# Kernel optimization log

Hardware: AMD Instinct MI355X
Metric: run time of the kernel (lower is better)

## Reference

```python
import jax, jax.numpy as jnp
import numpy as np

H = 8
D_MODEL = 512
NEG = -1e9  # fp32 masking value from the torch source


def setup_inputs() -> dict:
    key = jax.random.key(0)
    ks = jax.random.split(key, 13)
    B, T, C, D = 2, 512, 8, D_MODEL
    s = 1.0 / np.sqrt(D)
    inp = {
        "query": jax.random.normal(ks[0], (B, T, C, D), jnp.float32),
        "key": jax.random.normal(ks[1], (B, T, C, D), jnp.float32),
        "value": jax.random.normal(ks[2], (B, T, C, D), jnp.float32),
        "mask": jax.random.randint(ks[3], (B, T, T, 1), 0, 2, jnp.int32),
        # four Linear(d_model, d_model) layers, stored as (in, out)
        "Wq": jax.random.normal(ks[4], (D, D), jnp.float32) * s,
        "bq": jax.random.normal(ks[5], (D,), jnp.float32) * s,
        "Wk": jax.random.normal(ks[6], (D, D), jnp.float32) * s,
        "bk": jax.random.normal(ks[7], (D,), jnp.float32) * s,
        "Wv": jax.random.normal(ks[8], (D, D), jnp.float32) * s,
        "bv": jax.random.normal(ks[9], (D,), jnp.float32) * s,
        "Wo": jax.random.normal(ks[10], (D, D), jnp.float32) * s,
        "bo": jax.random.normal(ks[11], (D,), jnp.float32) * s,
    }
    return inp


def _mha(query, key, value, mask, Wq, bq, Wk, bk, Wv, bv, Wo, bo):
    B, T, C, D = query.shape
    h, dk = H, D // H

    def proj(x, W, b):
        y = (x @ W + b).reshape(B, T, C, h, dk)
        return jnp.transpose(y, (0, 3, 2, 1, 4))  # [B,h,C,T,dk] (torch transpose(1,3))

    q = proj(query, Wq, bq)
    k = proj(key, Wk, bk)
    v = proj(value, Wv, bv)

    scores = jnp.einsum("bhctd,bhcsd->bhcts", q, k) / np.sqrt(dk)  # [B,h,C,T,T]
    # The torch view/transpose/view dance is just a permutation putting C last;
    # it is equivalent to masking scores[b,h,c,t,s] where mask[b,t,s,0]==0
    # (mask broadcast over heads h and channels c).
    m = mask[:, :, :, 0]  # [B,T,Tk]
    scores = jnp.where(m[:, None, None, :, :] == 0, NEG, scores)
    p_attn = jax.nn.softmax(scores, axis=-1)
    # dropout omitted (inference/deterministic reference)
    x = jnp.einsum("bhcts,bhcsd->bhctd", p_attn, v)  # [B,h,C,T,dk]
    x = jnp.transpose(x, (0, 3, 2, 1, 4)).reshape(B, T, C, D)
    return x @ Wo + bo


def reference(query, key, value, mask, Wq, bq, Wk, bk, Wv, bv, Wo, bo):
    return _mha(query, key, value, mask, Wq, bq, Wk, bk, Wv, bv, Wo, bo)
```

## Files before the change

kernel.cpp:

```cpp
#include <hip/hip_runtime.h>
#include <hip/hip_bf16.h>

typedef __bf16 bf16;
typedef __bf16 bf16x8 __attribute__((ext_vector_type(8)));
typedef float floatx4 __attribute__((ext_vector_type(4)));


#define AS1 __attribute__((address_space(1)))
#define AS3 __attribute__((address_space(3)))

__device__ __forceinline__ void gload_lds16(const bf16* g, bf16* l) {
    __builtin_amdgcn_global_load_lds((const AS1 unsigned int*)g,
                                     (AS3 unsigned int*)l, 16, 0, 0);
}

union Pack8 { bf16 h[8]; uint4 u; };
union Pack4 { bf16 h[4]; unsigned long long u; };

__global__ __launch_bounds__(256) void wtr_kernel(
    const float* __restrict__ Wq, const float* __restrict__ Wk,
    const float* __restrict__ Wv, const float* __restrict__ Wo,
    bf16* __restrict__ WT)
{
    __shared__ float Ts[64][65];
    const int tid = threadIdx.x;
    const int k0 = blockIdx.x * 64;
    const int n0 = blockIdx.y * 64;
    const int z  = blockIdx.z;
    const float* W = (z == 0) ? Wq : (z == 1) ? Wk : (z == 2) ? Wv : Wo;
    bf16* O = WT + (size_t)z * 512 * 512;
    #pragma unroll
    for (int i = 0; i < 16; i++) {
        const int r = i * 4 + (tid >> 6), c = tid & 63;
        Ts[r][c] = W[(size_t)(k0 + r) * 512 + n0 + c];
    }
    __syncthreads();
    #pragma unroll
    for (int i = 0; i < 16; i++) {
        const int a = i * 4 + (tid >> 6), c = tid & 63;
        O[(size_t)(n0 + a) * 512 + k0 + c] = (bf16)Ts[c][a];
    }
}

__global__ __launch_bounds__(512, 4) void gemm_qkv(
    const float* __restrict__ Aq, const float* __restrict__ Ak,
    const float* __restrict__ Av, const bf16* __restrict__ WT,
    const float* __restrict__ Bq, const float* __restrict__ Bk,
    const float* __restrict__ Bv,
    bf16* __restrict__ Oq, bf16* __restrict__ Ok, bf16* __restrict__ Ov)
{
    __shared__ bf16 Asm[128 * 32];
    __shared__ bf16 Bsm[128 * 32];
    __shared__ bf16 Tsm[128][136];
    const int z = blockIdx.z;
    const float* A    = (z == 0) ? Aq : (z == 1) ? Ak : Av;
    const float* bias = (z == 0) ? Bq : (z == 1) ? Bk : Bv;
    bf16* out         = (z == 0) ? Oq : (z == 1) ? Ok : Ov;
    const bf16* BT = WT + (size_t)z * 262144;
    const float scale = (z == 0) ? 0.125f : 1.0f;

    const int tid  = threadIdx.x;
    const int lane = tid & 63;
    const int wave = tid >> 6;
    const int quad = lane >> 4;
    const int l16  = lane & 15;
    const int mblk = blockIdx.x * 128;
    const int nblk = blockIdx.y * 128;

    const int srow = wave * 16 + (lane >> 2);
    const int scol = (lane & 3) * 8;
    const float* Ag = A + (size_t)(mblk + srow) * 512 + scol;
    const bf16* Bg  = BT + (size_t)(nblk + srow) * 512 + scol;
    bf16* Alp = Asm + srow * 32 + scol;
    bf16* Bl  = Bsm + wave * 16 * 32;

    const int wr = (wave >> 1) * 32;
    const int wc = (wave & 1) * 64;

    floatx4 acc[2][4] = {};
    for (int k0 = 0; k0 < 512; k0 += 32) {
        gload_lds16(Bg + k0, Bl);
        float4 x0 = *(const float4*)(Ag + k0);
        float4 x1 = *(const float4*)(Ag + k0 + 4);
        Pack8 pa;
        pa.h[0] = (bf16)x0.x; pa.h[1] = (bf16)x0.y;
        pa.h[2] = (bf16)x0.z; pa.h[3] = (bf16)x0.w;
        pa.h[4] = (bf16)x1.x; pa.h[5] = (bf16)x1.y;
        pa.h[6] = (bf16)x1.z; pa.h[7] = (bf16)x1.w;
        *(uint4*)Alp = pa.u;
        __syncthreads();
        bf16x8 a[2], b[4];
        #pragma unroll
        for (int mt = 0; mt < 2; mt++)
            a[mt] = *(const bf16x8*)(Asm + (wr + mt * 16 + l16) * 32 + quad * 8);
        #pragma unroll
        for (int nt = 0; nt < 4; nt++)
            b[nt] = *(const bf16x8*)(Bsm + (wc + nt * 16 + l16) * 32 + quad * 8);
        #pragma unroll
        for (int mt = 0; mt < 2; mt++)
            #pragma unroll
            for (int nt = 0; nt < 4; nt++)
                acc[mt][nt] = __builtin_amdgcn_mfma_f32_16x16x32_bf16(
                    a[mt], b[nt], acc[mt][nt], 0, 0, 0);
        __syncthreads();
    }

    if (z != 2) {
        #pragma unroll
        for (int mt = 0; mt < 2; mt++) {
            #pragma unroll
            for (int nt = 0; nt < 4; nt++) {
                const int colg = nblk + wc + nt * 16 + l16;
                const float bb = bias[colg];
                #pragma unroll
                for (int r = 0; r < 4; r++) {
                    const int rowg = mblk + wr + mt * 16 + quad * 4 + r;
                    const float v = (acc[mt][nt][r] + bb) * scale;
                    const int b_ = rowg >> 12;
                    const int t_ = (rowg >> 3) & 511;
                    const int c  = rowg & 7;
                    const int h  = colg >> 6;
                    const int d  = colg & 63;
                    const int hd = b_ * 64 + h * 8 + c;
                    out[((size_t)hd * 512 + t_) * 64 + d] = (bf16)v;
                }
            }
        }
    } else {
        #pragma unroll
        for (int mt = 0; mt < 2; mt++) {
            #pragma unroll
            for (int nt = 0; nt < 4; nt++) {
                const int cl = wc + nt * 16 + l16;
                const float bb = bias[nblk + cl];
                #pragma unroll
                for (int r = 0; r < 4; r++)
                    Tsm[wr + mt * 16 + quad * 4 + r][cl] =
                        (bf16)(acc[mt][nt][r] + bb);
            }
        }
        __syncthreads();
        const int b_ = mblk >> 12;
        const int t0 = (mblk >> 3) & 511;
        #pragma unroll
        for (int ch = tid; ch < 1024; ch += 512) {
            const int col = ch >> 3, c = ch & 7;
            const int h = (nblk + col) >> 6, d = (nblk + col) & 63;
            const int hd = b_ * 64 + h * 8 + c;
            Pack8 lo, hi;
            #pragma unroll
            for (int j = 0; j < 8; j++) lo.h[j] = Tsm[j * 8 + c][col];
            #pragma unroll
            for (int j = 0; j < 8; j++) hi.h[j] = Tsm[(j + 8) * 8 + c][col];
            bf16* dst = out + ((size_t)hd * 64 + d) * 512 + t0;
            *(uint4*)dst = lo.u;
            *(uint4*)(dst + 8) = hi.u;
        }
    }
}

__global__ __launch_bounds__(512, 4) void gemm_o(
    const bf16* __restrict__ A, const bf16* __restrict__ BT,
    const float* __restrict__ bias, float* __restrict__ out)
{
    __shared__ bf16 Asm[128 * 32];
    __shared__ bf16 Bsm[128 * 32];
    const int tid  = threadIdx.x;
    const int lane = tid & 63;
    const int wave = tid >> 6;
    const int quad = lane >> 4;
    const int l16  = lane & 15;
    const int mblk = blockIdx.x * 128;
    const int nblk = blockIdx.y * 128;

    const int srow = wave * 16 + (lane >> 2);
    const int scol = (lane & 3) * 8;
    const bf16* Ag = A + (size_t)(mblk + srow) * 512 + scol;
    const bf16* Bg = BT + (size_t)(nblk + srow) * 512 + scol;
    bf16* Al = Asm + wave * 16 * 32;
    bf16* Bl = Bsm + wave * 16 * 32;

    const int wr = (wave >> 1) * 32;
    const int wc = (wave & 1) * 64;

    floatx4 acc[2][4] = {};
    for (int k0 = 0; k0 < 512; k0 += 32) {
        gload_lds16(Ag + k0, Al);
        gload_lds16(Bg + k0, Bl);
        __syncthreads();
        bf16x8 a[2], b[4];
        #pragma unroll
        for (int mt = 0; mt < 2; mt++)
            a[mt] = *(const bf16x8*)(Asm + (wr + mt * 16 + l16) * 32 + quad * 8);
        #pragma unroll
        for (int nt = 0; nt < 4; nt++)
            b[nt] = *(const bf16x8*)(Bsm + (wc + nt * 16 + l16) * 32 + quad * 8);
        #pragma unroll
        for (int mt = 0; mt < 2; mt++)
            #pragma unroll
            for (int nt = 0; nt < 4; nt++)
                acc[mt][nt] = __builtin_amdgcn_mfma_f32_16x16x32_bf16(
                    a[mt], b[nt], acc[mt][nt], 0, 0, 0);
        __syncthreads();
    }

    #pragma unroll
    for (int mt = 0; mt < 2; mt++) {
        #pragma unroll
        for (int nt = 0; nt < 4; nt++) {
            const int colg = nblk + wc + nt * 16 + l16;
            const float bb = bias[colg];
            #pragma unroll
            for (int r = 0; r < 4; r++) {
                const int rowg = mblk + wr + mt * 16 + quad * 4 + r;
                out[(size_t)rowg * 512 + colg] = acc[mt][nt][r] + bb;
            }
        }
    }
}

#define PST 520

__global__ __launch_bounds__(256, 2) void attn_kernel(
    const bf16* __restrict__ Qws, const bf16* __restrict__ Kws,
    const bf16* __restrict__ Vtws, const int* __restrict__ mask,
    bf16* __restrict__ Xws)
{
    __shared__ bf16 Psm[64][PST];
    __shared__ float redM[4][64];
    __shared__ float redS[4][64];
    const int tid  = threadIdx.x;
    const int wave = tid >> 6;
    const int lane = tid & 63;
    const int quad = lane >> 4;
    const int l16  = lane & 15;
    const int s_ = blockIdx.x;
    const int o_ = ((s_ & 7) << 7) | (s_ >> 3);
    const int hd = o_ >> 3;
    const int qt = o_ & 7;
    const int q0 = qt * 64;
    const int b = hd >> 6;
    const int h = (hd >> 3) & 7;
    const int c = hd & 7;

    const bf16* Qh = Qws + (size_t)hd * 512 * 64;
    const bf16* Kh = Kws + (size_t)hd * 512 * 64;
    const int* mp = mask + ((size_t)b * 512 + q0) * 512;

    bf16x8 aq[4][2];
    #pragma unroll
    for (int s = 0; s < 4; s++) {
        aq[s][0] = *(const bf16x8*)(Qh + (size_t)(q0 + s * 16 + l16) * 64 + quad * 8);
        aq[s][1] = *(const bf16x8*)(Qh + (size_t)(q0 + s * 16 + l16) * 64 + 32 + quad * 8);
    }

    floatx4 sv[4][8];
    #pragma unroll
    for (int s = 0; s < 4; s++)
        #pragma unroll
        for (int nt = 0; nt < 8; nt++)
            sv[s][nt] = (floatx4){0.f, 0.f, 0.f, 0.f};

    #pragma unroll
    for (int nt = 0; nt < 8; nt++) {
        const int s0 = wave * 128 + nt * 16;
        bf16x8 bk0 = *(const bf16x8*)(Kh + (size_t)(s0 + l16) * 64 + quad * 8);
        bf16x8 bk1 = *(const bf16x8*)(Kh + (size_t)(s0 + l16) * 64 + 32 + quad * 8);
        #pragma unroll
        for (int s = 0; s < 4; s++) {
            sv[s][nt] = __builtin_amdgcn_mfma_f32_16x16x32_bf16(
                bk0, aq[s][0], sv[s][nt], 0, 0, 0);
            sv[s][nt] = __builtin_amdgcn_mfma_f32_16x16x32_bf16(
                bk1, aq[s][1], sv[s][nt], 0, 0, 0);
        }
    }

    float mx[4] = {-3.0e38f, -3.0e38f, -3.0e38f, -3.0e38f};
    #pragma unroll
    for (int s = 0; s < 4; s++)
        #pragma unroll
        for (int nt = 0; nt < 8; nt++) {
            const int4 mv = *(const int4*)(
                mp + (size_t)(s * 16 + l16) * 512 + wave * 128 + nt * 16 + quad * 4);
            float v0 = sv[s][nt][0] + ((mv.x == 0) ? -1.0e9f : 0.0f);
            float v1 = sv[s][nt][1] + ((mv.y == 0) ? -1.0e9f : 0.0f);
            float v2 = sv[s][nt][2] + ((mv.z == 0) ? -1.0e9f : 0.0f);
            float v3 = sv[s][nt][3] + ((mv.w == 0) ? -1.0e9f : 0.0f);
            sv[s][nt][0] = v0; sv[s][nt][1] = v1;
            sv[s][nt][2] = v2; sv[s][nt][3] = v3;
            mx[s] = fmaxf(mx[s], fmaxf(fmaxf(v0, v1), fmaxf(v2, v3)));
        }
    #pragma unroll
    for (int s = 0; s < 4; s++) {
        mx[s] = fmaxf(mx[s], __shfl_xor(mx[s], 16, 64));
        mx[s] = fmaxf(mx[s], __shfl_xor(mx[s], 32, 64));
    }
    if (quad == 0)
        #pragma unroll
        for (int s = 0; s < 4; s++) redM[wave][s * 16 + l16] = mx[s];
    __syncthreads();

    float mf[4], sum[4] = {0.f, 0.f, 0.f, 0.f};
    #pragma unroll
    for (int s = 0; s < 4; s++) {
        const int qr = s * 16 + l16;
        mf[s] = fmaxf(fmaxf(redM[0][qr], redM[1][qr]),
                      fmaxf(redM[2][qr], redM[3][qr]));
    }
    #pragma unroll
    for (int s = 0; s < 4; s++)
        #pragma unroll
        for (int nt = 0; nt < 8; nt++)
            #pragma unroll
            for (int r = 0; r < 4; r++) {
                const float e = __expf(sv[s][nt][r] - mf[s]);
                sv[s][nt][r] = e;
                sum[s] += e;
            }
    #pragma unroll
    for (int s = 0; s < 4; s++) {
        sum[s] += __shfl_xor(sum[s], 16, 64);
        sum[s] += __shfl_xor(sum[s], 32, 64);
    }
    if (quad == 0)
        #pragma unroll
        for (int s = 0; s < 4; s++) redS[wave][s * 16 + l16] = sum[s];
    __syncthreads();

    float inv[4];
    #pragma unroll
    for (int s = 0; s < 4; s++) {
        const int qr = s * 16 + l16;
        inv[s] = 1.f / (redS[0][qr] + redS[1][qr] + redS[2][qr] + redS[3][qr]);
    }
    #pragma unroll
    for (int s = 0; s < 4; s++)
        #pragma unroll
        for (int nt = 0; nt < 8; nt++) {
            Pack4 pk;
            #pragma unroll
            for (int r = 0; r < 4; r++)
                pk.h[r] = (bf16)(sv[s][nt][r] * inv[s]);
            *(unsigned long long*)&Psm[s * 16 + l16][wave * 128 + nt * 16 + quad * 4]
                = pk.u;
        }
    __syncthreads();

    const bf16* Vh = Vtws + (size_t)hd * 64 * 512;
    const int d0 = wave * 16;
    floatx4 o[4] = {};
    #pragma unroll
    for (int ks = 0; ks < 16; ks++) {
        bf16x8 bv = *(const bf16x8*)(Vh + (size_t)(d0 + l16) * 512 + ks * 32 + quad * 8);
        #pragma unroll
        for (int rt = 0; rt < 4; rt++) {
            bf16x8 ap = *(const bf16x8*)(&Psm[rt * 16 + l16][ks * 32 + quad * 8]);
            o[rt] = __builtin_amdgcn_mfma_f32_16x16x32_bf16(ap, bv, o[rt], 0, 0, 0);
        }
    }
    #pragma unroll
    for (int rt = 0; rt < 4; rt++)
        #pragma unroll
        for (int r = 0; r < 4; r++) {
            const int q = q0 + rt * 16 + quad * 4 + r;
            const size_t row = ((size_t)b * 512 + q) * 8 + c;
            Xws[row * 512 + h * 64 + d0 + l16] = (bf16)o[rt][r];
        }
}

extern "C" void kernel_launch(void* const* d_in, const int* in_sizes, int n_in,
                              void* d_out, int out_size, void* d_ws, size_t ws_size,
                              hipStream_t stream)
{
    const float* qin  = (const float*)d_in[0];
    const float* kin  = (const float*)d_in[1];
    const float* vin  = (const float*)d_in[2];
    const int*   mask = (const int*)d_in[3];
    const float* Bq = (const float*)d_in[5];
    const float* Bk = (const float*)d_in[7];
    const float* Bv = (const float*)d_in[9];
    const float* Bo = (const float*)d_in[11];
    float* out = (float*)d_out;

    const size_t R = (size_t)8192 * 512;
    bf16* r0 = (bf16*)d_ws;
    bf16* r1 = r0 + R;
    bf16* r2 = r1 + R;
    bf16* r3 = r2 + R;
    bf16* WT = r3 + R;

    wtr_kernel<<<dim3(8, 8, 4), dim3(256), 0, stream>>>(
        (const float*)d_in[4], (const float*)d_in[6],
        (const float*)d_in[8], (const float*)d_in[10], WT);
    gemm_qkv<<<dim3(64, 4, 3), dim3(512), 0, stream>>>(
        qin, kin, vin, WT, Bq, Bk, Bv, r0, r1, r2);
    attn_kernel<<<dim3(1024), dim3(256), 0, stream>>>(
        r0, r1, r2, mask, r3);
    gemm_o<<<dim3(64, 4), dim3(512), 0, stream>>>(
        r3, WT + (size_t)3 * 262144, Bo, out);
}
```

Measured before the change: 193.5 us.

## Double-buffer LDS and register-prefetch tiles in QKV and output GEMMs

Replaces the single-buffered global_load_lds loop in both projection GEMMs with a fully unrolled, double-buffered LDS pipeline. Global loads for tile t+2 are issued into registers while tile t is computed, and custom lgkmcnt+barrier asm replaces __syncthreads. The aim is to hide global-load latency behind MFMA work. In exchange it uses more LDS and registers, and it drops the direct-to-LDS loads in favour of register staging.

```diff
diff --git a/kernel.cpp b/kernel.cpp
--- a/kernel.cpp
+++ b/kernel.cpp
@@ -6,16 +6,17 @@
 typedef float floatx4 __attribute__((ext_vector_type(4)));
 
 
-#define AS1 __attribute__((address_space(1)))
-#define AS3 __attribute__((address_space(3)))
-
-__device__ __forceinline__ void gload_lds16(const bf16* g, bf16* l) {
-    __builtin_amdgcn_global_load_lds((const AS1 unsigned int*)g,
-                                     (AS3 unsigned int*)l, 16, 0, 0);
-}
-
 union Pack8 { bf16 h[8]; uint4 u; };
 union Pack4 { bf16 h[4]; unsigned long long u; };
+
+__device__ __forceinline__ void store_pack8(bf16* dst, float4 a, float4 b) {
+    Pack8 p;
+    p.h[0] = (bf16)a.x; p.h[1] = (bf16)a.y; p.h[2] = (bf16)a.z; p.h[3] = (bf16)a.w;
+    p.h[4] = (bf16)b.x; p.h[5] = (bf16)b.y; p.h[6] = (bf16)b.z; p.h[7] = (bf16)b.w;
+    *(uint4*)dst = p.u;
+}
+
+#define BAR_LG asm volatile("s_waitcnt lgkmcnt(0)\n\ts_barrier" ::: "memory")
 
 __global__ __launch_bounds__(256) void wtr_kernel(
     const float* __restrict__ Wq, const float* __restrict__ Wk,
@@ -49,9 +50,12 @@
     const float* __restrict__ Bv,
     bf16* __restrict__ Oq, bf16* __restrict__ Ok, bf16* __restrict__ Ov)
 {
-    __shared__ bf16 Asm[128 * 32];
-    __shared__ bf16 Bsm[128 * 32];
-    __shared__ bf16 Tsm[128][136];
+    __shared__ __align__(16) bf16 smem[17408];
+    bf16* Ab0 = smem;
+    bf16* Ab1 = smem + 4096;
+    bf16* Bb0 = smem + 8192;
+    bf16* Bb1 = smem + 12288;
+
     const int z = blockIdx.z;
     const float* A    = (z == 0) ? Aq : (z == 1) ? Ak : Av;
     const float* bias = (z == 0) ? Bq : (z == 1) ? Bk : Bv;
@@ -71,38 +75,68 @@
     const int scol = (lane & 3) * 8;
     const float* Ag = A + (size_t)(mblk + srow) * 512 + scol;
     const bf16* Bg  = BT + (size_t)(nblk + srow) * 512 + scol;
-    bf16* Alp = Asm + srow * 32 + scol;
-    bf16* Bl  = Bsm + wave * 16 * 32;
+    const int aoff = srow * 32 + scol;
 
     const int wr = (wave >> 1) * 32;
     const int wc = (wave & 1) * 64;
 
     floatx4 acc[2][4] = {};
-    for (int k0 = 0; k0 < 512; k0 += 32) {
-        gload_lds16(Bg + k0, Bl);
-        float4 x0 = *(const float4*)(Ag + k0);
-        float4 x1 = *(const float4*)(Ag + k0 + 4);
-        Pack8 pa;
-        pa.h[0] = (bf16)x0.x; pa.h[1] = (bf16)x0.y;
-        pa.h[2] = (bf16)x0.z; pa.h[3] = (bf16)x0.w;
-        pa.h[4] = (bf16)x1.x; pa.h[5] = (bf16)x1.y;
-        pa.h[6] = (bf16)x1.z; pa.h[7] = (bf16)x1.w;
-        *(uint4*)Alp = pa.u;
-        __syncthreads();
+
+    float4 ax0 = *(const float4*)(Ag);
+    float4 ax1 = *(const float4*)(Ag + 4);
+    uint4  bx  = *(const uint4*)(Bg);
+    store_pack8(Ab0 + aoff, ax0, ax1);
+    *(uint4*)(Bb0 + aoff) = bx;
+    float4 ay0 = *(const float4*)(Ag + 32);
+    float4 ay1 = *(const float4*)(Ag + 36);
+    uint4  by  = *(const uint4*)(Bg + 32);
+    store_pack8(Ab1 + aoff, ay0, ay1);
+    *(uint4*)(Bb1 + aoff) = by;
+    ax0 = *(const float4*)(Ag + 64);
+    ax1 = *(const float4*)(Ag + 68);
+    bx  = *(const uint4*)(Bg + 64);
+    BAR_LG;
+
+    #pragma unroll
+    for (int t = 0; t < 16; t++) {
+        bf16* Ab = (t & 1) ? Ab1 : Ab0;
+        bf16* Bb = (t & 1) ? Bb1 : Bb0;
         bf16x8 a[2], b[4];
         #pragma unroll
         for (int mt = 0; mt < 2; mt++)
-            a[mt] = *(const bf16x8*)(Asm + (wr + mt * 16 + l16) * 32 + quad * 8);
+            a[mt] = *(const bf16x8*)(Ab + (wr + mt * 16 + l16) * 32 + quad * 8);
         #pragma unroll
         for (int nt = 0; nt < 4; nt++)
-            b[nt] = *(const bf16x8*)(Bsm + (wc + nt * 16 + l16) * 32 + quad * 8);
+            b[nt] = *(const bf16x8*)(Bb + (wc + nt * 16 + l16) * 32 + quad * 8);
         #pragma unroll
         for (int mt = 0; mt < 2; mt++)
             #pragma unroll
             for (int nt = 0; nt < 4; nt++)
                 acc[mt][nt] = __builtin_amdgcn_mfma_f32_16x16x32_bf16(
                     a[mt], b[nt], acc[mt][nt], 0, 0, 0);
-        __syncthreads();
+        if (t <= 12) {
+            const int kL = (t + 3) * 32;
+            if (t & 1) {
+                ax0 = *(const float4*)(Ag + kL);
+                ax1 = *(const float4*)(Ag + kL + 4);
+                bx  = *(const uint4*)(Bg + kL);
+            } else {
+                ay0 = *(const float4*)(Ag + kL);
+                ay1 = *(const float4*)(Ag + kL + 4);
+                by  = *(const uint4*)(Bg + kL);
+            }
+        }
+        if (t <= 13) {
+            BAR_LG;
+            if (t & 1) {
+                store_pack8(Ab + aoff, ay0, ay1);
+                *(uint4*)(Bb + aoff) = by;
+            } else {
+                store_pack8(Ab + aoff, ax0, ax1);
+                *(uint4*)(Bb + aoff) = bx;
+            }
+            BAR_LG;
+        }
     }
 
     if (z != 2) {
@@ -127,6 +161,9 @@
             }
         }
     } else {
+        __syncthreads();
+        typedef bf16 TsmRow[136];
+        TsmRow* Tsm = (TsmRow*)smem;
         #pragma unroll
         for (int mt = 0; mt < 2; mt++) {
             #pragma unroll
@@ -163,8 +200,12 @@
     const bf16* __restrict__ A, const bf16* __restrict__ BT,
     const float* __restrict__ bias, float* __restrict__ out)
 {
-    __shared__ bf16 Asm[128 * 32];
-    __shared__ bf16 Bsm[128 * 32];
+    __shared__ __align__(16) bf16 smem[16384];
+    bf16* Ab0 = smem;
+    bf16* Ab1 = smem + 4096;
+    bf16* Bb0 = smem + 8192;
+    bf16* Bb1 = smem + 12288;
+
     const int tid  = threadIdx.x;
     const int lane = tid & 63;
     const int wave = tid >> 6;
@@ -177,31 +218,53 @@
     const int scol = (lane & 3) * 8;
     const bf16* Ag = A + (size_t)(mblk + srow) * 512 + scol;
     const bf16* Bg = BT + (size_t)(nblk + srow) * 512 + scol;
-    bf16* Al = Asm + wave * 16 * 32;
-    bf16* Bl = Bsm + wave * 16 * 32;
+    const int aoff = srow * 32 + scol;
 
     const int wr = (wave >> 1) * 32;
     const int wc = (wave & 1) * 64;
 
     floatx4 acc[2][4] = {};
-    for (int k0 = 0; k0 < 512; k0 += 32) {
-        gload_lds16(Ag + k0, Al);
-        gload_lds16(Bg + k0, Bl);
-        __syncthreads();
+
+    uint4 xa = *(const uint4*)(Ag);
+    uint4 xb = *(const uint4*)(Bg);
+    *(uint4*)(Ab0 + aoff) = xa;
+    *(uint4*)(Bb0 + aoff) = xb;
+    uint4 ya = *(const uint4*)(Ag + 32);
+    uint4 yb = *(const uint4*)(Bg + 32);
+    *(uint4*)(Ab1 + aoff) = ya;
+    *(uint4*)(Bb1 + aoff) = yb;
+    xa = *(const uint4*)(Ag + 64);
+    xb = *(const uint4*)(Bg + 64);
+    BAR_LG;
+
+    #pragma unroll
+    for (int t = 0; t < 16; t++) {
+        bf16* Ab = (t & 1) ? Ab1 : Ab0;
+        bf16* Bb = (t & 1) ? Bb1 : Bb0;
         bf16x8 a[2], b[4];
         #pragma unroll
         for (int mt = 0; mt < 2; mt++)
-            a[mt] = *(const bf16x8*)(Asm + (wr + mt * 16 + l16) * 32 + quad * 8);
+            a[mt] = *(const bf16x8*)(Ab + (wr + mt * 16 + l16) * 32 + quad * 8);
         #pragma unroll
         for (int nt = 0; nt < 4; nt++)
-            b[nt] = *(const bf16x8*)(Bsm + (wc + nt * 16 + l16) * 32 + quad * 8);
+            b[nt] = *(const bf16x8*)(Bb + (wc + nt * 16 + l16) * 32 + quad * 8);
         #pragma unroll
         for (int mt = 0; mt < 2; mt++)
             #pragma unroll
             for (int nt = 0; nt < 4; nt++)
                 acc[mt][nt] = __builtin_amdgcn_mfma_f32_16x16x32_bf16(
                     a[mt], b[nt], acc[mt][nt], 0, 0, 0);
-        __syncthreads();
+        if (t <= 12) {
+            const int kL = (t + 3) * 32;
+            if (t & 1) { xa = *(const uint4*)(Ag + kL); xb = *(const uint4*)(Bg + kL); }
+            else       { ya = *(const uint4*)(Ag + kL); yb = *(const uint4*)(Bg + kL); }
+        }
+        if (t <= 13) {
+            BAR_LG;
+            if (t & 1) { *(uint4*)(Ab + aoff) = ya; *(uint4*)(Bb + aoff) = yb; }
+            else       { *(uint4*)(Ab + aoff) = xa; *(uint4*)(Bb + aoff) = xb; }
+            BAR_LG;
+        }
     }
 
     #pragma unroll
```

Measured after the change: 195.4 us. No clear change (+1.0%).

## Retile QKV GEMM to full-width 64-row blocks and shrink output GEMM tiles

Applied to the files above, without the earlier changes.

The QKV projection now gives each block 64 rows across all 512 output columns. Each fp32 input row is therefore read and converted to bf16 once instead of four times. The V transpose epilogue is staged through a shared buffer reused in four column chunks. The output GEMM switches to 64x128 tiles with 256 threads, doubling the block count for better CU occupancy. The risks are more accumulator registers per thread, lower occupancy from the larger shared footprint, and extra syncs in the V epilogue.

```diff
diff --git a/kernel.cpp b/kernel.cpp
--- a/kernel.cpp
+++ b/kernel.cpp
@@ -16,6 +16,12 @@
 
 union Pack8 { bf16 h[8]; uint4 u; };
 union Pack4 { bf16 h[4]; unsigned long long u; };
+
+__device__ __forceinline__ void store_pack4(bf16* dst, float4 a) {
+    Pack4 p;
+    p.h[0] = (bf16)a.x; p.h[1] = (bf16)a.y; p.h[2] = (bf16)a.z; p.h[3] = (bf16)a.w;
+    *(unsigned long long*)dst = p.u;
+}
 
 __global__ __launch_bounds__(256) void wtr_kernel(
     const float* __restrict__ Wq, const float* __restrict__ Wk,
@@ -42,16 +48,17 @@
     }
 }
 
-__global__ __launch_bounds__(512, 4) void gemm_qkv(
+__global__ __launch_bounds__(512, 3) void gemm_qkv(
     const float* __restrict__ Aq, const float* __restrict__ Ak,
     const float* __restrict__ Av, const bf16* __restrict__ WT,
     const float* __restrict__ Bq, const float* __restrict__ Bk,
     const float* __restrict__ Bv,
     bf16* __restrict__ Oq, bf16* __restrict__ Ok, bf16* __restrict__ Ov)
 {
-    __shared__ bf16 Asm[128 * 32];
-    __shared__ bf16 Bsm[128 * 32];
-    __shared__ bf16 Tsm[128][136];
+    __shared__ __align__(16) bf16 smem[18432];
+    bf16* Asm = smem;
+    bf16* Bsm = smem + 2048;
+
     const int z = blockIdx.z;
     const float* A    = (z == 0) ? Aq : (z == 1) ? Ak : Av;
     const float* bias = (z == 0) ? Bq : (z == 1) ? Bk : Bv;
@@ -64,40 +71,36 @@
     const int wave = tid >> 6;
     const int quad = lane >> 4;
     const int l16  = lane & 15;
-    const int mblk = blockIdx.x * 128;
-    const int nblk = blockIdx.y * 128;
-
-    const int srow = wave * 16 + (lane >> 2);
-    const int scol = (lane & 3) * 8;
-    const float* Ag = A + (size_t)(mblk + srow) * 512 + scol;
-    const bf16* Bg  = BT + (size_t)(nblk + srow) * 512 + scol;
-    bf16* Alp = Asm + srow * 32 + scol;
-    bf16* Bl  = Bsm + wave * 16 * 32;
-
-    const int wr = (wave >> 1) * 32;
-    const int wc = (wave & 1) * 64;
-
-    floatx4 acc[2][4] = {};
+    const int mblk = blockIdx.x * 64;
+
+    const int arow = tid >> 3;
+    const int acol = (tid & 7) * 4;
+    const float* Ag = A + (size_t)(mblk + arow) * 512 + acol;
+    const int aoff = arow * 32 + acol;
+    const int srowB = wave * 16 + (lane >> 2);
+    const int scolB = (lane & 3) * 8;
+    const bf16* Bg = BT + (size_t)srowB * 512 + scolB;
+    bf16* Bl = Bsm + wave * 16 * 32;
+
+    const int wc = wave * 64;
+
+    floatx4 acc[4][4] = {};
     for (int k0 = 0; k0 < 512; k0 += 32) {
-        gload_lds16(Bg + k0, Bl);
-        float4 x0 = *(const float4*)(Ag + k0);
-        float4 x1 = *(const float4*)(Ag + k0 + 4);
-        Pack8 pa;
-        pa.h[0] = (bf16)x0.x; pa.h[1] = (bf16)x0.y;
-        pa.h[2] = (bf16)x0.z; pa.h[3] = (bf16)x0.w;
-        pa.h[4] = (bf16)x1.x; pa.h[5] = (bf16)x1.y;
-        pa.h[6] = (bf16)x1.z; pa.h[7] = (bf16)x1.w;
-        *(uint4*)Alp = pa.u;
+        #pragma unroll
+        for (int i = 0; i < 4; i++)
+            gload_lds16(Bg + (size_t)i * 128 * 512 + k0, Bl + i * 128 * 32);
+        float4 x = *(const float4*)(Ag + k0);
+        store_pack4(Asm + aoff, x);
         __syncthreads();
-        bf16x8 a[2], b[4];
-        #pragma unroll
-        for (int mt = 0; mt < 2; mt++)
-            a[mt] = *(const bf16x8*)(Asm + (wr + mt * 16 + l16) * 32 + quad * 8);
+        bf16x8 a[4], b[4];
+        #pragma unroll
+        for (int mt = 0; mt < 4; mt++)
+            a[mt] = *(const bf16x8*)(Asm + (mt * 16 + l16) * 32 + quad * 8);
         #pragma unroll
         for (int nt = 0; nt < 4; nt++)
             b[nt] = *(const bf16x8*)(Bsm + (wc + nt * 16 + l16) * 32 + quad * 8);
         #pragma unroll
-        for (int mt = 0; mt < 2; mt++)
+        for (int mt = 0; mt < 4; mt++)
             #pragma unroll
             for (int nt = 0; nt < 4; nt++)
                 acc[mt][nt] = __builtin_amdgcn_mfma_f32_16x16x32_bf16(
@@ -107,14 +110,14 @@
 
     if (z != 2) {
         #pragma unroll
-        for (int mt = 0; mt < 2; mt++) {
+        for (int mt = 0; mt < 4; mt++) {
             #pragma unroll
             for (int nt = 0; nt < 4; nt++) {
-                const int colg = nblk + wc + nt * 16 + l16;
+                const int colg = wc + nt * 16 + l16;
                 const float bb = bias[colg];
                 #pragma unroll
                 for (int r = 0; r < 4; r++) {
-                    const int rowg = mblk + wr + mt * 16 + quad * 4 + r;
+                    const int rowg = mblk + mt * 16 + quad * 4 + r;
                     const float v = (acc[mt][nt][r] + bb) * scale;
                     const int b_ = rowg >> 12;
                     const int t_ = (rowg >> 3) & 511;
@@ -127,66 +130,76 @@
             }
         }
     } else {
-        #pragma unroll
-        for (int mt = 0; mt < 2; mt++) {
-            #pragma unroll
-            for (int nt = 0; nt < 4; nt++) {
-                const int cl = wc + nt * 16 + l16;
-                const float bb = bias[nblk + cl];
-                #pragma unroll
-                for (int r = 0; r < 4; r++)
-                    Tsm[wr + mt * 16 + quad * 4 + r][cl] =
-                        (bf16)(acc[mt][nt][r] + bb);
-            }
-        }
         __syncthreads();
+        typedef bf16 TsmRow[136];
+        TsmRow* Tsm = (TsmRow*)smem;
         const int b_ = mblk >> 12;
         const int t0 = (mblk >> 3) & 511;
         #pragma unroll
-        for (int ch = tid; ch < 1024; ch += 512) {
-            const int col = ch >> 3, c = ch & 7;
-            const int h = (nblk + col) >> 6, d = (nblk + col) & 63;
-            const int hd = b_ * 64 + h * 8 + c;
-            Pack8 lo, hi;
-            #pragma unroll
-            for (int j = 0; j < 8; j++) lo.h[j] = Tsm[j * 8 + c][col];
-            #pragma unroll
-            for (int j = 0; j < 8; j++) hi.h[j] = Tsm[(j + 8) * 8 + c][col];
-            bf16* dst = out + ((size_t)hd * 64 + d) * 512 + t0;
-            *(uint4*)dst = lo.u;
-            *(uint4*)(dst + 8) = hi.u;
-        }
-    }
-}
-
-__global__ __launch_bounds__(512, 4) void gemm_o(
+        for (int cb = 0; cb < 4; cb++) {
+            if ((wave >> 1) == cb) {
+                #pragma unroll
+                for (int mt = 0; mt < 4; mt++) {
+                    #pragma unroll
+                    for (int nt = 0; nt < 4; nt++) {
+                        const int colg = wc + nt * 16 + l16;
+                        const int cl = colg - cb * 128;
+                        const float bb = bias[colg];
+                        #pragma unroll
+                        for (int r = 0; r < 4; r++)
+                            Tsm[mt * 16 + quad * 4 + r][cl] =
+                                (bf16)(acc[mt][nt][r] + bb);
+                    }
+                }
+            }
+            __syncthreads();
+            #pragma unroll
+            for (int e = tid; e < 1024; e += 512) {
+                const int col = e >> 3, c = e & 7;
+                const int gcol = cb * 128 + col;
+                const int h = gcol >> 6, d = gcol & 63;
+                const int hd = b_ * 64 + h * 8 + c;
+                Pack8 pk;
+                #pragma unroll
+                for (int j = 0; j < 8; j++) pk.h[j] = Tsm[j * 8 + c][col];
+                *(uint4*)(out + ((size_t)hd * 64 + d) * 512 + t0) = pk.u;
+            }
+            __syncthreads();
+        }
+    }
+}
+
+__global__ __launch_bounds__(256) void gemm_o(
     const bf16* __restrict__ A, const bf16* __restrict__ BT,
     const float* __restrict__ bias, float* __restrict__ out)
 {
-    __shared__ bf16 Asm[128 * 32];
+    __shared__ bf16 Asm[64 * 32];
     __shared__ bf16 Bsm[128 * 32];
     const int tid  = threadIdx.x;
     const int lane = tid & 63;
     const int wave = tid >> 6;
     const int quad = lane >> 4;
     const int l16  = lane & 15;
-    const int mblk = blockIdx.x * 128;
+    const int mblk = blockIdx.x * 64;
     const int nblk = blockIdx.y * 128;
 
     const int srow = wave * 16 + (lane >> 2);
     const int scol = (lane & 3) * 8;
-    const bf16* Ag = A + (size_t)(mblk + srow) * 512 + scol;
-    const bf16* Bg = BT + (size_t)(nblk + srow) * 512 + scol;
-    bf16* Al = Asm + wave * 16 * 32;
-    bf16* Bl = Bsm + wave * 16 * 32;
+    const bf16* Ag  = A + (size_t)(mblk + srow) * 512 + scol;
+    const bf16* Bg0 = BT + (size_t)(nblk + srow) * 512 + scol;
+    const bf16* Bg1 = Bg0 + (size_t)64 * 512;
+    bf16* Al  = Asm + wave * 16 * 32;
+    bf16* Bl0 = Bsm + wave * 16 * 32;
+    bf16* Bl1 = Bsm + (64 + wave * 16) * 32;
 
     const int wr = (wave >> 1) * 32;
     const int wc = (wave & 1) * 64;
 
     floatx4 acc[2][4] = {};
     for (int k0 = 0; k0 < 512; k0 += 32) {
-        gload_lds16(Ag + k0, Al);
-        gload_lds16(Bg + k0, Bl);
+        gload_lds16(Ag + k0,  Al);
+        gload_lds16(Bg0 + k0, Bl0);
+        gload_lds16(Bg1 + k0, Bl1);
         __syncthreads();
         bf16x8 a[2], b[4];
         #pragma unroll
@@ -392,10 +405,10 @@
     wtr_kernel<<<dim3(8, 8, 4), dim3(256), 0, stream>>>(
         (const float*)d_in[4], (const float*)d_in[6],
         (const float*)d_in[8], (const float*)d_in[10], WT);
-    gemm_qkv<<<dim3(64, 4, 3), dim3(512), 0, stream>>>(
+    gemm_qkv<<<dim3(128, 1, 3), dim3(512), 0, stream>>>(
         qin, kin, vin, WT, Bq, Bk, Bv, r0, r1, r2);
     attn_kernel<<<dim3(1024), dim3(256), 0, stream>>>(
         r0, r1, r2, mask, r3);
-    gemm_o<<<dim3(64, 4), dim3(512), 0, stream>>>(
+    gemm_o<<<dim3(128, 4), dim3(256), 0, stream>>>(
         r3, WT + (size_t)3 * 262144, Bo, out);
 }
```

Result: no change. 190.4 us (-1.6%).
